# Kernel optimization log

Hardware: AMD Instinct MI355X
Metric: run time of the kernel (lower is better)

The kernel has to match this reference:

```python
import jax, jax.numpy as jnp
import numpy as np

EMBED_SIZE = 1024
HEADS = 16
HEAD_DIM = EMBED_SIZE // HEADS  # 64


def setup_inputs() -> dict:
    key = jax.random.key(0)
    k_x, k_q, k_k, k_v, k_o, k_b = jax.random.split(key, 6)
    B, S = 32, 8192  # S divisible by HEADS
    x = jax.random.normal(k_x, (B, S, HEAD_DIM), dtype=jnp.float32)
    # torch.nn.Linear weights are [out, in]; scale ~ 1/sqrt(fan_in)
    s_h = 1.0 / np.sqrt(HEAD_DIM)
    s_e = 1.0 / np.sqrt(EMBED_SIZE)
    Wq = jax.random.uniform(k_q, (HEAD_DIM, HEAD_DIM), jnp.float32, -s_h, s_h)
    Wk = jax.random.uniform(k_k, (HEAD_DIM, HEAD_DIM), jnp.float32, -s_h, s_h)
    Wv = jax.random.uniform(k_v, (HEAD_DIM, HEAD_DIM), jnp.float32, -s_h, s_h)
    Wo = jax.random.uniform(k_o, (EMBED_SIZE, EMBED_SIZE), jnp.float32, -s_e, s_e)
    bo = jax.random.uniform(k_b, (EMBED_SIZE,), jnp.float32, -s_e, s_e)
    return {"x": x, "Wq": Wq, "Wk": Wk, "Wv": Wv, "Wo": Wo, "bo": bo}


def reference(x, Wq, Wk, Wv, Wo, bo):
    B = x.shape[0]
    # Q/K/V projections: Linear(head_dim, head_dim), bias=False -> x @ W.T
    Q = (x @ Wq.T).reshape(B, -1, HEADS, HEAD_DIM)  # [B, G, H, D], G = S/H
    K = (x @ Wk.T).reshape(B, -1, HEADS, HEAD_DIM)
    V = (x @ Wv.T).reshape(B, -1, HEADS, HEAD_DIM)
    # energy = Q @ K^T over last two dims -> [B, G, H, H]
    energy = jnp.einsum('bghd,bgkd->bghk', Q, K)
    attn = jax.nn.softmax(energy / jnp.sqrt(jnp.float32(EMBED_SIZE)), axis=3)
    out = jnp.einsum('bghk,bgkd->bghd', attn, V)      # [B, G, H, D]
    out = out.transpose(0, 2, 1, 3).reshape(B, -1, EMBED_SIZE)  # [B, S/H, E]
    return out @ Wo.T + bo
```

## Files before the change

kernel.cpp:

```cpp
#include <hip/hip_runtime.h>
#include <hip/hip_bf16.h>
#include <stdint.h>

#define TOKS   262144
#define NGRP   16384
#define EMB    1024
#define HD     64

using bf16x8 = __attribute__((ext_vector_type(8))) short;
using f32x4  = __attribute__((ext_vector_type(4))) float;

__device__ __forceinline__ unsigned pack2(float a, float b) {
    union { __hip_bfloat162 h; unsigned u; } cvt;
    cvt.h = __float22bfloat162_rn(make_float2(a, b));
    return cvt.u;
}
__device__ __forceinline__ bf16x8 cvt8(float4 v0, float4 v1) {
    uint4 u;
    u.x = pack2(v0.x, v0.y);
    u.y = pack2(v0.z, v0.w);
    u.z = pack2(v1.x, v1.y);
    u.w = pack2(v1.z, v1.w);
    return __builtin_bit_cast(bf16x8, u);
}
__device__ __forceinline__ void gload_lds16(const unsigned short* g, unsigned short* l) {
    __builtin_amdgcn_global_load_lds(
        (const __attribute__((address_space(1))) void*)g,
        (__attribute__((address_space(3))) void*)l,
        16, 0, 0);
}

__global__ __launch_bounds__(256) void k_cvt(const float* __restrict__ wo,
                                             const float* __restrict__ wq,
                                             const float* __restrict__ wk,
                                             const float* __restrict__ wv,
                                             unsigned short* __restrict__ wob,
                                             unsigned short* __restrict__ wqkvb) {
    int bid = blockIdx.x;
    if (bid < 1024) {
        int idx = (bid * 256 + threadIdx.x) * 4;
        float4 v = *(const float4*)(wo + idx);
        uint2 p;
        p.x = pack2(v.x, v.y);
        p.y = pack2(v.z, v.w);
        *(uint2*)(wob + idx) = p;
    } else {
        int b = bid - 1024;
        int m = b >> 2;
        const float* src = (m == 0) ? wq : ((m == 1) ? wk : wv);
        int idx = ((b & 3) * 256 + threadIdx.x) * 4;
        float4 v = *(const float4*)(src + idx);
        uint2 p;
        p.x = pack2(v.x, v.y);
        p.y = pack2(v.z, v.w);
        *(uint2*)(wqkvb + m * 4096 + idx) = p;
    }
}

#define SCL 0.0450842200278f

__global__ __launch_bounds__(256) void k_fused(const float* __restrict__ x,
                                               const unsigned short* __restrict__ wqkv,
                                               unsigned short* __restrict__ out2) {
    __shared__ __align__(16) unsigned short qkls[4][2][2][16 * 72];
    int t = threadIdx.x;
    int w = t >> 6, l = t & 63;
    int c = l & 15, q = l >> 4;
    int waveTok0 = blockIdx.x * 128 + w * 32;

    bf16x8 xa[2][2];
    #pragma unroll
    for (int g = 0; g < 2; ++g) {
        const float* xp = x + (size_t)(waveTok0 + g * 16 + c) * 64 + q * 8;
        #pragma unroll
        for (int kc = 0; kc < 2; ++kc) {
            float4 v0 = *(const float4*)(xp + kc * 32);
            float4 v1 = *(const float4*)(xp + kc * 32 + 4);
            xa[g][kc] = cvt8(v0, v1);
        }
    }

    uint2 pkV[2][4];
    #pragma unroll
    for (int m = 0; m < 3; ++m) {
        #pragma unroll
        for (int nb = 0; nb < 4; ++nb) {
            const unsigned short* wp = wqkv + m * 4096 + (nb * 16 + c) * 64 + q * 8;
            bf16x8 w0 = *(const bf16x8*)(wp);
            bf16x8 w1 = *(const bf16x8*)(wp + 32);
            #pragma unroll
            for (int g = 0; g < 2; ++g) {
                f32x4 acc = (f32x4){0.f, 0.f, 0.f, 0.f};
                acc = __builtin_amdgcn_mfma_f32_16x16x32_bf16(xa[g][0], w0, acc, 0, 0, 0);
                acc = __builtin_amdgcn_mfma_f32_16x16x32_bf16(xa[g][1], w1, acc, 0, 0, 0);
                unsigned u01 = pack2(acc[0], acc[1]);
                unsigned u23 = pack2(acc[2], acc[3]);
                if (m < 2) {
                    unsigned short* tile = qkls[w][g][m];
                    int base = 4 * q * 72 + nb * 16 + c;
                    tile[base]       = (unsigned short)u01;
                    tile[base + 72]  = (unsigned short)(u01 >> 16);
                    tile[base + 144] = (unsigned short)u23;
                    tile[base + 216] = (unsigned short)(u23 >> 16);
                } else {
                    pkV[g][nb].x = u01;
                    pkV[g][nb].y = u23;
                }
            }
        }
    }

    f32x4 e[2];
    #pragma unroll
    for (int g = 0; g < 2; ++g) {
        const unsigned short* Qt = qkls[w][g][0];
        const unsigned short* Kt = qkls[w][g][1];
        e[g] = (f32x4){0.f, 0.f, 0.f, 0.f};
        #pragma unroll
        for (int kc = 0; kc < 2; ++kc) {
            bf16x8 ka = *(const bf16x8*)(Kt + c * 72 + kc * 32 + q * 8);
            bf16x8 qb = *(const bf16x8*)(Qt + c * 72 + kc * 32 + q * 8);
            e[g] = __builtin_amdgcn_mfma_f32_16x16x32_bf16(ka, qb, e[g], 0, 0, 0);
        }
    }

    unsigned pa0[2], pa1[2];
    #pragma unroll
    for (int g = 0; g < 2; ++g) {
        float mx = fmaxf(fmaxf(e[g][0], e[g][1]), fmaxf(e[g][2], e[g][3]));
        mx = fmaxf(mx, __shfl_xor(mx, 16));
        mx = fmaxf(mx, __shfl_xor(mx, 32));
        float p0 = exp2f((e[g][0] - mx) * SCL);
        float p1 = exp2f((e[g][1] - mx) * SCL);
        float p2 = exp2f((e[g][2] - mx) * SCL);
        float p3 = exp2f((e[g][3] - mx) * SCL);
        float s = p0 + p1 + p2 + p3;
        s += __shfl_xor(s, 16);
        s += __shfl_xor(s, 32);
        float rinv = 1.0f / s;
        pa0[g] = pack2(p0 * rinv, p1 * rinv);
        pa1[g] = pack2(p2 * rinv, p3 * rinv);
    }

    int s0 = (32 * q + c) & 63;
    int s1 = (32 * q + 16 + c) & 63;
    int v0 = 32 * (q & 1) + c;
    int v1 = v0 + 16;
    bool hi = (q >= 2);
    #pragma unroll
    for (int g = 0; g < 2; ++g) {
        int a0 = __shfl((int)pa0[g], s0);
        int a1 = __shfl((int)pa1[g], s0);
        int a2 = __shfl((int)pa0[g], s1);
        int a3 = __shfl((int)pa1[g], s1);
        uint4 A2u;
        A2u.x = hi ? 0u : (unsigned)a0;
        A2u.y = hi ? 0u : (unsigned)a1;
        A2u.z = hi ? 0u : (unsigned)a2;
        A2u.w = hi ? 0u : (unsigned)a3;
        bf16x8 A2 = __builtin_bit_cast(bf16x8, A2u);

        unsigned short* Ot = qkls[w][g][0];
        #pragma unroll
        for (int nb = 0; nb < 4; ++nb) {
            uint4 B2u;
            B2u.x = (unsigned)__shfl((int)pkV[g][nb].x, v0);
            B2u.y = (unsigned)__shfl((int)pkV[g][nb].y, v0);
            B2u.z = (unsigned)__shfl((int)pkV[g][nb].x, v1);
            B2u.w = (unsigned)__shfl((int)pkV[g][nb].y, v1);
            bf16x8 B2 = __builtin_bit_cast(bf16x8, B2u);
            f32x4 o = (f32x4){0.f, 0.f, 0.f, 0.f};
            o = __builtin_amdgcn_mfma_f32_16x16x32_bf16(A2, B2, o, 0, 0, 0);
            unsigned u01 = pack2(o[0], o[1]);
            unsigned u23 = pack2(o[2], o[3]);
            int base = 4 * q * 72 + nb * 16 + c;
            Ot[base]       = (unsigned short)u01;
            Ot[base + 72]  = (unsigned short)(u01 >> 16);
            Ot[base + 144] = (unsigned short)u23;
            Ot[base + 216] = (unsigned short)(u23 >> 16);
        }
    }

    #pragma unroll
    for (int g = 0; g < 2; ++g) {
        int gi = (waveTok0 >> 4) + g;
        int b    = gi >> 9;
        int grem = gi & 511;
        int rowbase = b * 512 + (grem >> 4);
        int colpref = (grem & 15) * 64;
        const unsigned short* osrc = qkls[w][g][0] + (l >> 2) * 72 + (l & 3) * 16;
        uint4 ov0 = *(const uint4*)(osrc);
        uint4 ov1 = *(const uint4*)(osrc + 8);
        unsigned short* dst = out2 + (size_t)(rowbase + (l >> 2) * 32) * 1024
                                   + colpref + (l & 3) * 16;
        *(uint4*)(dst)     = ov0;
        *(uint4*)(dst + 8) = ov1;
    }
}

__global__ __launch_bounds__(256) void k_gemm(const unsigned short* __restrict__ A,
                                              const unsigned short* __restrict__ Bm,
                                              const float* __restrict__ bias,
                                              float* __restrict__ C) {
    __shared__ __align__(16) unsigned short As[128 * 64];
    __shared__ __align__(16) unsigned short Bs[128 * 64];
    const int K = 1024;
    int t  = threadIdx.x;
    int id = blockIdx.x;
    int m0 = (id & 127) * 128;
    int n0 = (id >> 7) * 128;
    int w  = t >> 6;
    int l  = t & 63;
    int wm = (w & 1) * 64;
    int wn = (w >> 1) * 64;
    int lm = l & 15;
    int q4 = l >> 4;
    int jxor = lm & 7;

    const unsigned short* Ag[4];
    const unsigned short* Bg[4];
    #pragma unroll
    for (int qq = 0; qq < 4; ++qq) {
        int s   = t + 256 * qq;
        int row = s >> 3;
        int jg  = (s & 7) ^ (row & 7);
        Ag[qq] = A  + (size_t)(m0 + row) * K + jg * 8;
        Bg[qq] = Bm + (size_t)(n0 + row) * K + jg * 8;
    }

    f32x4 acc[4][4];
    #pragma unroll
    for (int mi = 0; mi < 4; ++mi)
        #pragma unroll
        for (int ni = 0; ni < 4; ++ni)
            acc[mi][ni] = (f32x4){0.f, 0.f, 0.f, 0.f};

    for (int k0 = 0; k0 < K; k0 += 64) {
        #pragma unroll
        for (int qq = 0; qq < 4; ++qq) {
            gload_lds16(Ag[qq] + k0, As + (size_t)(t + 256 * qq) * 8);
            gload_lds16(Bg[qq] + k0, Bs + (size_t)(t + 256 * qq) * 8);
        }
        __syncthreads();

        #pragma unroll
        for (int kc = 0; kc < 2; ++kc) {
            int joff = ((kc * 4 + q4) ^ jxor) * 8;
            bf16x8 af[4], bfr[4];
            #pragma unroll
            for (int mi = 0; mi < 4; ++mi)
                af[mi] = *(const bf16x8*)(As + (wm + mi * 16 + lm) * 64 + joff);
            #pragma unroll
            for (int ni = 0; ni < 4; ++ni)
                bfr[ni] = *(const bf16x8*)(Bs + (wn + ni * 16 + lm) * 64 + joff);
            #pragma unroll
            for (int mi = 0; mi < 4; ++mi)
                #pragma unroll
                for (int ni = 0; ni < 4; ++ni)
                    acc[mi][ni] = __builtin_amdgcn_mfma_f32_16x16x32_bf16(
                        af[mi], bfr[ni], acc[mi][ni], 0, 0, 0);
        }
        __syncthreads();
    }

    #pragma unroll
    for (int mi = 0; mi < 4; ++mi) {
        #pragma unroll
        for (int ni = 0; ni < 4; ++ni) {
            int col = n0 + wn + ni * 16 + lm;
            float bcol = bias[col];
            #pragma unroll
            for (int r = 0; r < 4; ++r) {
                int row = m0 + wm + mi * 16 + q4 * 4 + r;
                C[(size_t)row * 1024 + col] = acc[mi][ni][r] + bcol;
            }
        }
    }
}

extern "C" void kernel_launch(void* const* d_in, const int* in_sizes, int n_in,
                              void* d_out, int out_size, void* d_ws, size_t ws_size,
                              hipStream_t stream) {
    const float* x  = (const float*)d_in[0];
    const float* wq = (const float*)d_in[1];
    const float* wk = (const float*)d_in[2];
    const float* wv = (const float*)d_in[3];
    const float* wo = (const float*)d_in[4];
    const float* bo = (const float*)d_in[5];
    float* out = (float*)d_out;

    unsigned short* out2  = (unsigned short*)d_ws;
    unsigned short* wob   = out2 + (size_t)NGRP * 1024;
    unsigned short* wqkvb = wob + (size_t)EMB * EMB;

    k_cvt  <<<1036, 256, 0, stream>>>(wo, wq, wk, wv, wob, wqkvb);
    k_fused<<<2048, 256, 0, stream>>>(x, wqkvb, out2);
    k_gemm <<<1024, 256, 0, stream>>>(out2, wob, bo, out);
}
```

Before: 178.1 us.

## Replace output GEMM with 256x256-tile double-buffered pipelined MFMA kernel

Result: no change. 177.1 us (-0.6%).

```diff
diff --git a/kernel.cpp b/kernel.cpp
--- a/kernel.cpp
+++ b/kernel.cpp
@@ -198,80 +198,162 @@
     }
 }
 
-__global__ __launch_bounds__(256) void k_gemm(const unsigned short* __restrict__ A,
-                                              const unsigned short* __restrict__ Bm,
-                                              const float* __restrict__ bias,
-                                              float* __restrict__ C) {
-    __shared__ __align__(16) unsigned short As[128 * 64];
-    __shared__ __align__(16) unsigned short Bs[128 * 64];
-    const int K = 1024;
-    int t  = threadIdx.x;
-    int id = blockIdx.x;
-    int m0 = (id & 127) * 128;
-    int n0 = (id >> 7) * 128;
-    int w  = t >> 6;
-    int l  = t & 63;
-    int wm = (w & 1) * 64;
-    int wn = (w >> 1) * 64;
-    int lm = l & 15;
-    int q4 = l >> 4;
-    int jxor = lm & 7;
-
-    const unsigned short* Ag[4];
-    const unsigned short* Bg[4];
-    #pragma unroll
-    for (int qq = 0; qq < 4; ++qq) {
-        int s   = t + 256 * qq;
-        int row = s >> 3;
-        int jg  = (s & 7) ^ (row & 7);
-        Ag[qq] = A  + (size_t)(m0 + row) * K + jg * 8;
-        Bg[qq] = Bm + (size_t)(n0 + row) * K + jg * 8;
-    }
-
-    f32x4 acc[4][4];
-    #pragma unroll
-    for (int mi = 0; mi < 4; ++mi)
+#define STG(gb, lb, half, kt) do { \
+    gload_lds16((gb) + (size_t)(half) * 131072 + (size_t)(kt) * 64 + ga0, \
+                (lb) + (half) * 8192 + lo0); \
+    gload_lds16((gb) + (size_t)(half) * 131072 + (size_t)(kt) * 64 + ga1, \
+                (lb) + (half) * 8192 + lo1); \
+} while (0)
+
+#define LDA4(buf, mh) do { \
+    _Pragma("unroll") \
+    for (int i2 = 0; i2 < 4; ++i2) { \
+        const unsigned short* _p = (buf) + (wrow + ((mh) * 4 + i2) * 16 + lm) * 64; \
+        a[i2][0] = *(const bf16x8*)(_p + jo0); \
+        a[i2][1] = *(const bf16x8*)(_p + jo1); \
+    } \
+} while (0)
+
+#define LDB2(dst, buf, nh) do { \
+    _Pragma("unroll") \
+    for (int j2 = 0; j2 < 2; ++j2) { \
+        const unsigned short* _p = (buf) + (wcol + ((nh) * 2 + j2) * 16 + lm) * 64; \
+        dst[j2][0] = *(const bf16x8*)(_p + jo0); \
+        dst[j2][1] = *(const bf16x8*)(_p + jo1); \
+    } \
+} while (0)
+
+#define MM8(mh, nh, B) do { \
+    _Pragma("unroll") \
+    for (int i2 = 0; i2 < 4; ++i2) { \
+        _Pragma("unroll") \
+        for (int j2 = 0; j2 < 2; ++j2) { \
+            acc[(mh)*4+i2][(nh)*2+j2] = __builtin_amdgcn_mfma_f32_16x16x32_bf16( \
+                a[i2][0], B[j2][0], acc[(mh)*4+i2][(nh)*2+j2], 0, 0, 0); \
+            acc[(mh)*4+i2][(nh)*2+j2] = __builtin_amdgcn_mfma_f32_16x16x32_bf16( \
+                a[i2][1], B[j2][1], acc[(mh)*4+i2][(nh)*2+j2], 0, 0, 0); \
+        } \
+    } \
+} while (0)
+
+#define PHASE_MID() do { \
+    __builtin_amdgcn_s_barrier(); \
+    asm volatile("s_waitcnt lgkmcnt(0)" ::: "memory"); \
+    __builtin_amdgcn_sched_barrier(0); \
+    __builtin_amdgcn_s_setprio(1); \
+} while (0)
+
+#define PHASE_END() do { \
+    __builtin_amdgcn_s_setprio(0); \
+    __builtin_amdgcn_s_barrier(); \
+} while (0)
+
+__global__ __launch_bounds__(512, 2) void k_gemm256(const unsigned short* __restrict__ A,
+                                                    const unsigned short* __restrict__ Bm,
+                                                    const float* __restrict__ bias,
+                                                    float* __restrict__ C) {
+    extern __shared__ __align__(16) unsigned short lds[];
+    unsigned short* As0 = lds;
+    unsigned short* As1 = lds + 16384;
+    unsigned short* Bs0 = lds + 32768;
+    unsigned short* Bs1 = lds + 49152;
+
+    const int t = threadIdx.x;
+    const int w = t >> 6, l = t & 63;
+    const int lm = l & 15, q4 = l >> 4;
+    const int jxor = lm & 7;
+    const int jo0 = ((0 + q4) ^ jxor) * 8;
+    const int jo1 = ((4 + q4) ^ jxor) * 8;
+
+    const int bid = blockIdx.x;
+    const int wg  = (bid & 7) * 32 + (bid >> 3);
+    const int m0  = (wg >> 2) * 256;
+    const int n0  = (wg & 3) * 256;
+
+    const int wrow = (w >> 2) * 128;
+    const int wcol = (w & 3) * 64;
+
+    const int s1 = w * 128 + l;
+    const int s2 = s1 + 64;
+    const int r0 = s1 >> 3, c0 = s1 & 7;
+    const int r1 = s2 >> 3, c1 = s2 & 7;
+    const size_t ga0 = (size_t)r0 * 1024 + (size_t)((c0 ^ (r0 & 7)) * 8);
+    const size_t ga1 = (size_t)r1 * 1024 + (size_t)((c1 ^ (r1 & 7)) * 8);
+    const int lo0 = s1 * 8;
+    const int lo1 = s2 * 8;
+
+    const unsigned short* Ab = A  + (size_t)m0 * 1024;
+    const unsigned short* Bb = Bm + (size_t)n0 * 1024;
+
+    f32x4 acc[8][4];
+    #pragma unroll
+    for (int mi = 0; mi < 8; ++mi)
         #pragma unroll
         for (int ni = 0; ni < 4; ++ni)
             acc[mi][ni] = (f32x4){0.f, 0.f, 0.f, 0.f};
 
-    for (int k0 = 0; k0 < K; k0 += 64) {
-        #pragma unroll
-        for (int qq = 0; qq < 4; ++qq) {
-            gload_lds16(Ag[qq] + k0, As + (size_t)(t + 256 * qq) * 8);
-            gload_lds16(Bg[qq] + k0, Bs + (size_t)(t + 256 * qq) * 8);
-        }
-        __syncthreads();
-
-        #pragma unroll
-        for (int kc = 0; kc < 2; ++kc) {
-            int joff = ((kc * 4 + q4) ^ jxor) * 8;
-            bf16x8 af[4], bfr[4];
-            #pragma unroll
-            for (int mi = 0; mi < 4; ++mi)
-                af[mi] = *(const bf16x8*)(As + (wm + mi * 16 + lm) * 64 + joff);
-            #pragma unroll
-            for (int ni = 0; ni < 4; ++ni)
-                bfr[ni] = *(const bf16x8*)(Bs + (wn + ni * 16 + lm) * 64 + joff);
-            #pragma unroll
-            for (int mi = 0; mi < 4; ++mi)
-                #pragma unroll
-                for (int ni = 0; ni < 4; ++ni)
-                    acc[mi][ni] = __builtin_amdgcn_mfma_f32_16x16x32_bf16(
-                        af[mi], bfr[ni], acc[mi][ni], 0, 0, 0);
-        }
-        __syncthreads();
-    }
-
-    #pragma unroll
-    for (int mi = 0; mi < 4; ++mi) {
-        #pragma unroll
-        for (int ni = 0; ni < 4; ++ni) {
-            int col = n0 + wn + ni * 16 + lm;
-            float bcol = bias[col];
+    bf16x8 a[4][2], b0[2][2], b1[2][2];
+
+    STG(Ab, As0, 0, 0); STG(Ab, As0, 1, 0);
+    STG(Bb, Bs0, 0, 0); STG(Bb, Bs0, 1, 0);
+    STG(Bb, Bs1, 0, 1); STG(Bb, Bs1, 1, 1);
+    asm volatile("s_waitcnt vmcnt(4)" ::: "memory");
+    __builtin_amdgcn_s_barrier();
+
+    #pragma unroll 1
+    for (int it = 0; it < 8; ++it) {
+        const int kt1 = 2 * it + 1;
+        const int kt2 = 2 * it + 2;
+        const int kt3 = 2 * it + 3;
+        const bool more = (it < 7);
+
+        LDA4(As0, 0); LDB2(b0, Bs0, 0);
+        STG(Ab, As1, 0, kt1);
+        PHASE_MID(); MM8(0, 0, b0); PHASE_END();
+
+        LDB2(b1, Bs0, 1);
+        STG(Ab, As1, 1, kt1);
+        PHASE_MID(); MM8(0, 1, b1); PHASE_END();
+
+        LDA4(As0, 1);
+        if (more) STG(Bb, Bs0, 0, kt2);
+        PHASE_MID(); MM8(1, 1, b1); PHASE_END();
+
+        if (more) STG(Bb, Bs0, 1, kt2);
+        PHASE_MID(); MM8(1, 0, b0);
+        __builtin_amdgcn_s_setprio(0);
+        if (more) { asm volatile("s_waitcnt vmcnt(4)" ::: "memory"); }
+        else      { asm volatile("s_waitcnt vmcnt(0)" ::: "memory"); }
+        __builtin_amdgcn_s_barrier();
+
+        LDA4(As1, 0); LDB2(b0, Bs1, 0);
+        if (more) STG(Ab, As0, 0, kt2);
+        PHASE_MID(); MM8(0, 0, b0); PHASE_END();
+
+        LDB2(b1, Bs1, 1);
+        if (more) STG(Ab, As0, 1, kt2);
+        PHASE_MID(); MM8(0, 1, b1); PHASE_END();
+
+        LDA4(As1, 1);
+        if (more) STG(Bb, Bs1, 0, kt3);
+        PHASE_MID(); MM8(1, 1, b1); PHASE_END();
+
+        if (more) STG(Bb, Bs1, 1, kt3);
+        PHASE_MID(); MM8(1, 0, b0);
+        __builtin_amdgcn_s_setprio(0);
+        if (more) { asm volatile("s_waitcnt vmcnt(4)" ::: "memory"); }
+        __builtin_amdgcn_s_barrier();
+    }
+
+    #pragma unroll
+    for (int ni = 0; ni < 4; ++ni) {
+        const int col = n0 + wcol + ni * 16 + lm;
+        const float bcol = bias[col];
+        #pragma unroll
+        for (int mi = 0; mi < 8; ++mi) {
             #pragma unroll
             for (int r = 0; r < 4; ++r) {
-                int row = m0 + wm + mi * 16 + q4 * 4 + r;
+                const int row = m0 + wrow + mi * 16 + q4 * 4 + r;
                 C[(size_t)row * 1024 + col] = acc[mi][ni][r] + bcol;
             }
         }
@@ -293,7 +375,14 @@
     unsigned short* wob   = out2 + (size_t)NGRP * 1024;
     unsigned short* wqkvb = wob + (size_t)EMB * EMB;
 
-    k_cvt  <<<1036, 256, 0, stream>>>(wo, wq, wk, wv, wob, wqkvb);
-    k_fused<<<2048, 256, 0, stream>>>(x, wqkvb, out2);
-    k_gemm <<<1024, 256, 0, stream>>>(out2, wob, bo, out);
-}
+    static int s_once = []() {
+        hipFuncSetAttribute((const void*)k_gemm256,
+                            hipFuncAttributeMaxDynamicSharedMemorySize, 131072);
+        return 0;
+    }();
+    (void)s_once;
+
+    k_cvt    <<<1036, 256, 0, stream>>>(wo, wq, wk, wv, wob, wqkvb);
+    k_fused  <<<2048, 256, 0, stream>>>(x, wqkvb, out2);
+    k_gemm256<<<256, 512, 131072, stream>>>(out2, wob, bo, out);
+}
```
